# Optimization experiments

Measured on AMD Instinct MI355X. Metric: run time of the kernel, lower is better.

The kernel has to match this reference:

```python
import jax, jax.numpy as jnp
import numpy as np

ALPHA_BASE = 1.2
ALPHA_SCALE = 0.3
GRAPH_LAMBDA = 0.3
FUSION_BETA = 0.1
PRIOR_BETA = 0.2
LN_EPS = 1e-5  # nn.LayerNorm default

B, L, C = 8, 8192, 512
STAT, HID, GF, EMB = 4, 16, 16, 16


def _linear_params(key, out_d, in_d):
    kw, kb = jax.random.split(key)
    bound = 1.0 / np.sqrt(in_d)
    W = jax.random.uniform(kw, (out_d, in_d), minval=-bound, maxval=bound, dtype=jnp.float32)
    b = jax.random.uniform(kb, (out_d,), minval=-bound, maxval=bound, dtype=jnp.float32)
    return W, b


def setup_inputs() -> dict:
    key = jax.random.key(0)
    ks = jax.random.split(key, 9)
    residual = jax.random.normal(ks[0], (B, L, C), dtype=jnp.float32)
    node_embedding = jax.random.normal(ks[1], (C, EMB), dtype=jnp.float32) * 0.02
    W_l1, b_l1 = _linear_params(ks[2], HID, STAT)
    W_l2, b_l2 = _linear_params(ks[3], HID, HID)
    W_g, b_g = _linear_params(ks[4], HID, STAT)
    W_q, b_q = _linear_params(ks[5], GF, STAT)
    W_k, b_k = _linear_params(ks[6], GF, STAT)
    W_f, b_f = _linear_params(ks[7], HID, HID)
    W_o, b_o = _linear_params(ks[8], 1, HID)
    ln_g = jnp.ones((HID,), jnp.float32)
    ln_b = jnp.zeros((HID,), jnp.float32)
    return dict(residual=residual, node_embedding=node_embedding,
                W_l1=W_l1, b_l1=b_l1, W_l2=W_l2, b_l2=b_l2,
                W_g=W_g, b_g=b_g, W_q=W_q, b_q=b_q, W_k=W_k, b_k=b_k,
                W_f=W_f, b_f=b_f, W_o=W_o, b_o=b_o, ln_g=ln_g, ln_b=ln_b)


def reference(residual, node_embedding, W_l1, b_l1, W_l2, b_l2, W_g, b_g,
              W_q, b_q, W_k, b_k, W_f, b_f, W_o, b_o, ln_g, ln_b):
    # --- residual statistics: [B,L,C] -> [B,C,4] ---
    abs_res = jnp.abs(residual)
    m = abs_res.mean(axis=1)                       # mean(|r|)
    mx = abs_res.max(axis=1)                       # max(|r|)
    sq = (residual * residual).mean(axis=1)        # energy == mean(|r|^2)
    std = jnp.sqrt(jnp.maximum(sq - m * m, 0.0))   # biased std of |r|
    h0 = jnp.stack([m, mx, std, sq], axis=-1)      # [B,C,4]

    # --- local branch ---
    h_local = jax.nn.relu(h0 @ W_l1.T + b_l1) @ W_l2.T + b_l2  # [B,C,H]

    # --- adaptive adjacency ---
    q = h0 @ W_q.T + b_q                            # [B,C,G]
    k = h0 @ W_k.T + b_k                            # [B,C,G]
    sim_data = jax.nn.relu(jnp.einsum('bcg,bdg->bcd', q, k))
    sim_prior = jax.nn.relu(node_embedding @ node_embedding.T)  # [C,C]
    eye = jnp.eye(sim_data.shape[-1], dtype=sim_data.dtype)
    sim = sim_data + PRIOR_BETA * sim_prior[None] + eye[None]
    A = jax.nn.softmax(sim, axis=-1)                # [B,C,C]

    # --- message passing ---
    h_graph_in = h0 @ W_g.T + b_g                   # [B,C,H]
    msg = jnp.einsum('bcd,bdh->bch', A, h_graph_in)
    h_graph = h_graph_in + GRAPH_LAMBDA * jax.nn.relu(msg)

    # --- fusion + layernorm + head ---
    h = h_local + FUSION_BETA * h_graph
    mu = h.mean(axis=-1, keepdims=True)
    var = ((h - mu) ** 2).mean(axis=-1, keepdims=True)
    h = (h - mu) / jnp.sqrt(var + LN_EPS) * ln_g + ln_b
    h = jax.nn.relu(h @ W_f.T + b_f)
    delta = ALPHA_SCALE * jnp.tanh(h @ W_o.T + b_o)  # [B,C,1]
    alpha = (ALPHA_BASE + delta).transpose(0, 2, 1)  # [B,1,C]
    return alpha, h0, A
```

## Files before the change

kernel.cpp:

```cpp
#include <hip/hip_runtime.h>
#include <math.h>

#define BB 8
#define LL 8192
#define CC 512
#define NCH 64

#define H0_OFF (BB*CC)
#define A_OFF  (H0_OFF + BB*CC*4)

#define F_ALPHA_BASE 1.2f
#define F_ALPHA_SCALE 0.3f
#define F_GRAPH_LAMBDA 0.3f
#define F_FUSION_BETA 0.1f
#define F_PRIOR_BETA 0.2f
#define F_LN_EPS 1e-5f

struct P {
    const float* res; const float* ne;
    const float* Wl1; const float* bl1; const float* Wl2; const float* bl2;
    const float* Wg;  const float* bg;  const float* Wq;  const float* bq;
    const float* Wk;  const float* bk;  const float* Wf;  const float* bf;
    const float* Wo;  const float* bo;  const float* lng; const float* lnb;
    float* out; float* pbuf;
};

__global__ __launch_bounds__(256) void k_stats(P p) {
    __shared__ float smem[3 * CC];
    int b = blockIdx.x >> 6, cb = blockIdx.x & 63;
    int sub = threadIdx.x >> 7;
    int c4 = (threadIdx.x & 127) * 4;
    const float* base = p.res + ((size_t)b * LL + cb * 128 + sub * 64) * CC + c4;
    float s0 = 0.f, s1 = 0.f, s2 = 0.f, s3 = 0.f;
    float m0 = 0.f, m1 = 0.f, m2 = 0.f, m3 = 0.f;
    float q0 = 0.f, q1 = 0.f, q2 = 0.f, q3 = 0.f;
    #pragma unroll 8
    for (int r = 0; r < 64; r++) {
        float4 v = *(const float4*)(base + (size_t)r * CC);
        s0 += fabsf(v.x); s1 += fabsf(v.y); s2 += fabsf(v.z); s3 += fabsf(v.w);
        m0 = fmaxf(m0, fabsf(v.x)); m1 = fmaxf(m1, fabsf(v.y));
        m2 = fmaxf(m2, fabsf(v.z)); m3 = fmaxf(m3, fabsf(v.w));
        q0 = fmaf(v.x, v.x, q0); q1 = fmaf(v.y, v.y, q1);
        q2 = fmaf(v.z, v.z, q2); q3 = fmaf(v.w, v.w, q3);
    }
    if (sub == 1) {
        *(float4*)&smem[0 * CC + c4] = make_float4(s0, s1, s2, s3);
        *(float4*)&smem[1 * CC + c4] = make_float4(m0, m1, m2, m3);
        *(float4*)&smem[2 * CC + c4] = make_float4(q0, q1, q2, q3);
    }
    __syncthreads();
    if (sub == 0) {
        float4 cs = *(const float4*)&smem[0 * CC + c4];
        float4 cm = *(const float4*)&smem[1 * CC + c4];
        float4 cq = *(const float4*)&smem[2 * CC + c4];
        s0 += cs.x; s1 += cs.y; s2 += cs.z; s3 += cs.w;
        m0 = fmaxf(m0, cm.x); m1 = fmaxf(m1, cm.y);
        m2 = fmaxf(m2, cm.z); m3 = fmaxf(m3, cm.w);
        q0 += cq.x; q1 += cq.y; q2 += cq.z; q3 += cq.w;
        float* pb = p.pbuf + ((size_t)(b * 3) * NCH + cb) * CC + c4;
        *(float4*)(pb)                        = make_float4(s0, s1, s2, s3);
        *(float4*)(pb + (size_t)NCH * CC)     = make_float4(m0, m1, m2, m3);
        *(float4*)(pb + (size_t)2 * NCH * CC) = make_float4(q0, q1, q2, q3);
    }
}

__global__ __launch_bounds__(256) void k_rows(P p) {
    __shared__ float pl[4 * CC];
    __shared__ float stg[3 * CC];
    int tid = threadIdx.x;
    int b = blockIdx.x >> 6, rb = blockIdx.x & 63;
    int wid = tid >> 6, lane = tid & 63;
    int row0 = rb * 8 + wid * 2;

    int c4 = (tid & 127) * 4;
    int part = tid >> 7;
    const float* pS = p.pbuf + ((size_t)(b * 3 + 0) * NCH + part * 32) * CC + c4;
    const float* pM = p.pbuf + ((size_t)(b * 3 + 1) * NCH + part * 32) * CC + c4;
    const float* pQ = p.pbuf + ((size_t)(b * 3 + 2) * NCH + part * 32) * CC + c4;
    float as0 = 0.f, as1 = 0.f, as2 = 0.f, as3 = 0.f;
    float am0 = 0.f, am1 = 0.f, am2 = 0.f, am3 = 0.f;
    float aq0 = 0.f, aq1 = 0.f, aq2 = 0.f, aq3 = 0.f;
    #pragma unroll 8
    for (int i = 0; i < 32; i++) {
        float4 v = *(const float4*)(pS + (size_t)i * CC);
        as0 += v.x; as1 += v.y; as2 += v.z; as3 += v.w;
        float4 w = *(const float4*)(pM + (size_t)i * CC);
        am0 = fmaxf(am0, w.x); am1 = fmaxf(am1, w.y);
        am2 = fmaxf(am2, w.z); am3 = fmaxf(am3, w.w);
        float4 u = *(const float4*)(pQ + (size_t)i * CC);
        aq0 += u.x; aq1 += u.y; aq2 += u.z; aq3 += u.w;
    }
    if (part == 1) {
        *(float4*)&stg[0 * CC + c4] = make_float4(as0, as1, as2, as3);
        *(float4*)&stg[1 * CC + c4] = make_float4(am0, am1, am2, am3);
        *(float4*)&stg[2 * CC + c4] = make_float4(aq0, aq1, aq2, aq3);
    }

    float nr[2][16];
    #pragma unroll
    for (int rr = 0; rr < 2; rr++) {
        #pragma unroll
        for (int t = 0; t < 4; t++) {
            float4 v = *(const float4*)(p.ne + (size_t)(row0 + rr) * 16 + t * 4);
            nr[rr][4 * t] = v.x; nr[rr][4 * t + 1] = v.y;
            nr[rr][4 * t + 2] = v.z; nr[rr][4 * t + 3] = v.w;
        }
    }
    float pr0[8], pr1[8];
    #pragma unroll
    for (int j = 0; j < 8; j++) {
        int col = lane + 64 * j;
        float d0 = 0.f, d1 = 0.f;
        #pragma unroll
        for (int t = 0; t < 4; t++) {
            float4 v = *(const float4*)(p.ne + (size_t)col * 16 + t * 4);
            d0 = fmaf(nr[0][4 * t], v.x, d0); d0 = fmaf(nr[0][4 * t + 1], v.y, d0);
            d0 = fmaf(nr[0][4 * t + 2], v.z, d0); d0 = fmaf(nr[0][4 * t + 3], v.w, d0);
            d1 = fmaf(nr[1][4 * t], v.x, d1); d1 = fmaf(nr[1][4 * t + 1], v.y, d1);
            d1 = fmaf(nr[1][4 * t + 2], v.z, d1); d1 = fmaf(nr[1][4 * t + 3], v.w, d1);
        }
        pr0[j] = fmaxf(d0, 0.f);
        pr1[j] = fmaxf(d1, 0.f);
    }

    __syncthreads();
    if (part == 0) {
        float4 cs = *(const float4*)&stg[0 * CC + c4];
        float4 cm = *(const float4*)&stg[1 * CC + c4];
        float4 cq = *(const float4*)&stg[2 * CC + c4];
        float S[4] = {as0 + cs.x, as1 + cs.y, as2 + cs.z, as3 + cs.w};
        float M[4] = {fmaxf(am0, cm.x), fmaxf(am1, cm.y), fmaxf(am2, cm.z), fmaxf(am3, cm.w)};
        float Q[4] = {aq0 + cq.x, aq1 + cq.y, aq2 + cq.z, aq3 + cq.w};
        #pragma unroll
        for (int k = 0; k < 4; k++) {
            float m = S[k] * (1.f / LL);
            float sqm = Q[k] * (1.f / LL);
            float sd = sqrtf(fmaxf(sqm - m * m, 0.f));
            int col = c4 + k;
            pl[col] = m;
            pl[CC + col] = M[k];
            pl[2 * CC + col] = sd;
            pl[3 * CC + col] = sqm;
            if (rb == 0)
                *(float4*)(p.out + H0_OFF + ((size_t)b * CC + col) * 4) =
                    make_float4(m, M[k], sd, sqm);
        }
    }
    __syncthreads();

    float sloc[2][4], u[2][4], c0[2];
    #pragma unroll
    for (int rr = 0; rr < 2; rr++) {
        int row = row0 + rr;
        float sv0 = pl[row], sv1 = pl[CC + row];
        float sv2 = pl[2 * CC + row], sv3 = pl[3 * CC + row];
        sloc[rr][0] = sv0; sloc[rr][1] = sv1; sloc[rr][2] = sv2; sloc[rr][3] = sv3;
        float uu0 = 0.f, uu1 = 0.f, uu2 = 0.f, uu3 = 0.f, cc = 0.f;
        #pragma unroll
        for (int i = 0; i < 16; i++) {
            float qi = p.bq[i];
            qi = fmaf(p.Wq[i * 4 + 0], sv0, qi);
            qi = fmaf(p.Wq[i * 4 + 1], sv1, qi);
            qi = fmaf(p.Wq[i * 4 + 2], sv2, qi);
            qi = fmaf(p.Wq[i * 4 + 3], sv3, qi);
            uu0 = fmaf(qi, p.Wk[i * 4 + 0], uu0);
            uu1 = fmaf(qi, p.Wk[i * 4 + 1], uu1);
            uu2 = fmaf(qi, p.Wk[i * 4 + 2], uu2);
            uu3 = fmaf(qi, p.Wk[i * 4 + 3], uu3);
            cc = fmaf(qi, p.bk[i], cc);
        }
        u[rr][0] = uu0; u[rr][1] = uu1; u[rr][2] = uu2; u[rr][3] = uu3;
        c0[rr] = cc;
    }

    float sv[2][8];
    float mx0 = -1e30f, mx1 = -1e30f;
    #pragma unroll
    for (int j = 0; j < 8; j++) {
        int col = lane + 64 * j;
        float h0c = pl[col], h1c = pl[CC + col];
        float h2c = pl[2 * CC + col], h3c = pl[3 * CC + col];
        float d0 = c0[0], d1 = c0[1];
        d0 = fmaf(u[0][0], h0c, d0); d1 = fmaf(u[1][0], h0c, d1);
        d0 = fmaf(u[0][1], h1c, d0); d1 = fmaf(u[1][1], h1c, d1);
        d0 = fmaf(u[0][2], h2c, d0); d1 = fmaf(u[1][2], h2c, d1);
        d0 = fmaf(u[0][3], h3c, d0); d1 = fmaf(u[1][3], h3c, d1);
        float v0 = fmaxf(d0, 0.f) + F_PRIOR_BETA * pr0[j] + (col == row0 ? 1.f : 0.f);
        float v1 = fmaxf(d1, 0.f) + F_PRIOR_BETA * pr1[j] + (col == row0 + 1 ? 1.f : 0.f);
        sv[0][j] = v0; sv[1][j] = v1;
        mx0 = fmaxf(mx0, v0); mx1 = fmaxf(mx1, v1);
    }
    #pragma unroll
    for (int o = 32; o; o >>= 1) {
        mx0 = fmaxf(mx0, __shfl_xor(mx0, o));
        mx1 = fmaxf(mx1, __shfl_xor(mx1, o));
    }

    float ls0 = 0.f, ls1 = 0.f;
    float T0[4] = {0.f, 0.f, 0.f, 0.f}, T1[4] = {0.f, 0.f, 0.f, 0.f};
    #pragma unroll
    for (int j = 0; j < 8; j++) {
        int col = lane + 64 * j;
        float e0 = expf(sv[0][j] - mx0);
        float e1 = expf(sv[1][j] - mx1);
        sv[0][j] = e0; sv[1][j] = e1;
        ls0 += e0; ls1 += e1;
        float h0c = pl[col], h1c = pl[CC + col];
        float h2c = pl[2 * CC + col], h3c = pl[3 * CC + col];
        T0[0] = fmaf(e0, h0c, T0[0]); T1[0] = fmaf(e1, h0c, T1[0]);
        T0[1] = fmaf(e0, h1c, T0[1]); T1[1] = fmaf(e1, h1c, T1[1]);
        T0[2] = fmaf(e0, h2c, T0[2]); T1[2] = fmaf(e1, h2c, T1[2]);
        T0[3] = fmaf(e0, h3c, T0[3]); T1[3] = fmaf(e1, h3c, T1[3]);
    }
    #pragma unroll
    for (int o = 32; o; o >>= 1) {
        ls0 += __shfl_xor(ls0, o); ls1 += __shfl_xor(ls1, o);
        T0[0] += __shfl_xor(T0[0], o); T1[0] += __shfl_xor(T1[0], o);
        T0[1] += __shfl_xor(T0[1], o); T1[1] += __shfl_xor(T1[1], o);
        T0[2] += __shfl_xor(T0[2], o); T1[2] += __shfl_xor(T1[2], o);
        T0[3] += __shfl_xor(T0[3], o); T1[3] += __shfl_xor(T1[3], o);
    }
    float inv0 = 1.f / ls0, inv1 = 1.f / ls1;

    float* arow = p.out + A_OFF + ((size_t)b * CC + row0) * CC;
    #pragma unroll
    for (int j = 0; j < 8; j++) {
        arow[lane + 64 * j]      = sv[0][j] * inv0;
        arow[CC + lane + 64 * j] = sv[1][j] * inv1;
    }

    int rr = lane >> 5;
    float inv = rr ? inv1 : inv0;
    float Ta = (rr ? T1[0] : T0[0]) * inv;
    float Tb = (rr ? T1[1] : T0[1]) * inv;
    float Tc = (rr ? T1[2] : T0[2]) * inv;
    float Td = (rr ? T1[3] : T0[3]) * inv;
    float s20 = rr ? sloc[1][0] : sloc[0][0];
    float s21 = rr ? sloc[1][1] : sloc[0][1];
    float s22 = rr ? sloc[1][2] : sloc[0][2];
    float s23 = rr ? sloc[1][3] : sloc[0][3];

    float gcomb[16];
    #pragma unroll
    for (int h = 0; h < 16; h++) {
        float w0 = p.Wg[h * 4 + 0], w1 = p.Wg[h * 4 + 1];
        float w2 = p.Wg[h * 4 + 2], w3 = p.Wg[h * 4 + 3];
        float bgh = p.bg[h];
        float hg = bgh;
        hg = fmaf(w0, s20, hg); hg = fmaf(w1, s21, hg);
        hg = fmaf(w2, s22, hg); hg = fmaf(w3, s23, hg);
        float mg = bgh;
        mg = fmaf(w0, Ta, mg); mg = fmaf(w1, Tb, mg);
        mg = fmaf(w2, Tc, mg); mg = fmaf(w3, Td, mg);
        gcomb[h] = hg + F_GRAPH_LAMBDA * fmaxf(mg, 0.f);
    }
    float t1v[16];
    #pragma unroll
    for (int i = 0; i < 16; i++) {
        float a = p.bl1[i];
        a = fmaf(p.Wl1[i * 4 + 0], s20, a);
        a = fmaf(p.Wl1[i * 4 + 1], s21, a);
        a = fmaf(p.Wl1[i * 4 + 2], s22, a);
        a = fmaf(p.Wl1[i * 4 + 3], s23, a);
        t1v[i] = fmaxf(a, 0.f);
    }
    float hvec[16];
    float mu = 0.f;
    #pragma unroll
    for (int h = 0; h < 16; h++) {
        float hl = p.bl2[h];
        #pragma unroll
        for (int j = 0; j < 16; j++) hl = fmaf(p.Wl2[h * 16 + j], t1v[j], hl);
        float hv = hl + F_FUSION_BETA * gcomb[h];
        hvec[h] = hv;
        mu += hv;
    }
    mu *= (1.f / 16.f);
    float var = 0.f;
    #pragma unroll
    for (int h = 0; h < 16; h++) { float d = hvec[h] - mu; var = fmaf(d, d, var); }
    var *= (1.f / 16.f);
    float istd = 1.f / sqrtf(var + F_LN_EPS);
    float hn[16];
    #pragma unroll
    for (int h = 0; h < 16; h++) hn[h] = (hvec[h] - mu) * istd * p.lng[h] + p.lnb[h];

    float acc2 = p.bo[0];
    #pragma unroll
    for (int o = 0; o < 16; o++) {
        float f = p.bf[o];
        #pragma unroll
        for (int t = 0; t < 16; t++) f = fmaf(p.Wf[o * 16 + t], hn[t], f);
        acc2 = fmaf(p.Wo[o], fmaxf(f, 0.f), acc2);
    }
    float alpha = F_ALPHA_BASE + F_ALPHA_SCALE * tanhf(acc2);
    if ((lane & 31) == 0) p.out[(size_t)b * CC + row0 + rr] = alpha;
}

extern "C" void kernel_launch(void* const* d_in, const int* in_sizes, int n_in,
                              void* d_out, int out_size, void* d_ws, size_t ws_size,
                              hipStream_t stream) {
    P p;
    p.res = (const float*)d_in[0];
    p.ne  = (const float*)d_in[1];
    p.Wl1 = (const float*)d_in[2];
    p.bl1 = (const float*)d_in[3];
    p.Wl2 = (const float*)d_in[4];
    p.bl2 = (const float*)d_in[5];
    p.Wg  = (const float*)d_in[6];
    p.bg  = (const float*)d_in[7];
    p.Wq  = (const float*)d_in[8];
    p.bq  = (const float*)d_in[9];
    p.Wk  = (const float*)d_in[10];
    p.bk  = (const float*)d_in[11];
    p.Wf  = (const float*)d_in[12];
    p.bf  = (const float*)d_in[13];
    p.Wo  = (const float*)d_in[14];
    p.bo  = (const float*)d_in[15];
    p.lng = (const float*)d_in[16];
    p.lnb = (const float*)d_in[17];
    p.out  = (float*)d_out;
    p.pbuf = (float*)d_ws;

    k_stats<<<BB * NCH, 256, 0, stream>>>(p);
    k_rows<<<BB * 64, 256, 0, stream>>>(p);
}
```

Measured before the change: 55.73 us.

## Hoist partial-stat reduction into a separate kernel shared by all row blocks

Adds a small k_red kernel that reduces the per-chunk sum/max/sumsq partials once per batch and channel, computes h0, and writes it to the output and a workspace buffer. k_rows now loads the precomputed h0 instead of each of its 64 blocks per batch redundantly re-reducing all partials. This removes heavy redundant L2/global reads at the cost of an extra kernel launch and a serial dependency.

```diff
diff --git a/kernel.cpp b/kernel.cpp
--- a/kernel.cpp
+++ b/kernel.cpp
@@ -22,7 +22,7 @@
     const float* Wg;  const float* bg;  const float* Wq;  const float* bq;
     const float* Wk;  const float* bk;  const float* Wf;  const float* bf;
     const float* Wo;  const float* bo;  const float* lng; const float* lnb;
-    float* out; float* pbuf;
+    float* out; float* pbuf; float* h0ws;
 };
 
 __global__ __launch_bounds__(256) void k_stats(P p) {
@@ -64,36 +64,55 @@
     }
 }
 
+__global__ __launch_bounds__(256) void k_red(P p) {
+    __shared__ float red[4][3][64];
+    int w = threadIdx.x >> 6, lane = threadIdx.x & 63;
+    int b = blockIdx.x >> 3;
+    int c = (blockIdx.x & 7) * 64 + lane;
+    const float* pS = p.pbuf + ((size_t)(b * 3 + 0) * NCH + w * 16) * CC + c;
+    const float* pM = p.pbuf + ((size_t)(b * 3 + 1) * NCH + w * 16) * CC + c;
+    const float* pQ = p.pbuf + ((size_t)(b * 3 + 2) * NCH + w * 16) * CC + c;
+    float sum = 0.f, mx = 0.f, sq = 0.f;
+    #pragma unroll
+    for (int i = 0; i < 16; i++) {
+        sum += pS[(size_t)i * CC];
+        mx = fmaxf(mx, pM[(size_t)i * CC]);
+        sq += pQ[(size_t)i * CC];
+    }
+    red[w][0][lane] = sum;
+    red[w][1][lane] = mx;
+    red[w][2][lane] = sq;
+    __syncthreads();
+    if (w == 0) {
+        float ts = red[0][0][lane] + red[1][0][lane] + red[2][0][lane] + red[3][0][lane];
+        float tm = fmaxf(fmaxf(red[0][1][lane], red[1][1][lane]),
+                         fmaxf(red[2][1][lane], red[3][1][lane]));
+        float tq = red[0][2][lane] + red[1][2][lane] + red[2][2][lane] + red[3][2][lane];
+        float m = ts * (1.f / LL);
+        float sqm = tq * (1.f / LL);
+        float sd = sqrtf(fmaxf(sqm - m * m, 0.f));
+        float4 h0v = make_float4(m, tm, sd, sqm);
+        size_t g = (size_t)b * CC + c;
+        *(float4*)(p.h0ws + g * 4) = h0v;
+        *(float4*)(p.out + H0_OFF + g * 4) = h0v;
+    }
+}
+
 __global__ __launch_bounds__(256) void k_rows(P p) {
     __shared__ float pl[4 * CC];
-    __shared__ float stg[3 * CC];
     int tid = threadIdx.x;
     int b = blockIdx.x >> 6, rb = blockIdx.x & 63;
     int wid = tid >> 6, lane = tid & 63;
     int row0 = rb * 8 + wid * 2;
 
-    int c4 = (tid & 127) * 4;
-    int part = tid >> 7;
-    const float* pS = p.pbuf + ((size_t)(b * 3 + 0) * NCH + part * 32) * CC + c4;
-    const float* pM = p.pbuf + ((size_t)(b * 3 + 1) * NCH + part * 32) * CC + c4;
-    const float* pQ = p.pbuf + ((size_t)(b * 3 + 2) * NCH + part * 32) * CC + c4;
-    float as0 = 0.f, as1 = 0.f, as2 = 0.f, as3 = 0.f;
-    float am0 = 0.f, am1 = 0.f, am2 = 0.f, am3 = 0.f;
-    float aq0 = 0.f, aq1 = 0.f, aq2 = 0.f, aq3 = 0.f;
-    #pragma unroll 8
-    for (int i = 0; i < 32; i++) {
-        float4 v = *(const float4*)(pS + (size_t)i * CC);
-        as0 += v.x; as1 += v.y; as2 += v.z; as3 += v.w;
-        float4 w = *(const float4*)(pM + (size_t)i * CC);
-        am0 = fmaxf(am0, w.x); am1 = fmaxf(am1, w.y);
-        am2 = fmaxf(am2, w.z); am3 = fmaxf(am3, w.w);
-        float4 u = *(const float4*)(pQ + (size_t)i * CC);
-        aq0 += u.x; aq1 += u.y; aq2 += u.z; aq3 += u.w;
-    }
-    if (part == 1) {
-        *(float4*)&stg[0 * CC + c4] = make_float4(as0, as1, as2, as3);
-        *(float4*)&stg[1 * CC + c4] = make_float4(am0, am1, am2, am3);
-        *(float4*)&stg[2 * CC + c4] = make_float4(aq0, aq1, aq2, aq3);
+    #pragma unroll
+    for (int ccy = 0; ccy < 2; ccy++) {
+        int col = tid + ccy * 256;
+        float4 hv = *(const float4*)(p.h0ws + ((size_t)b * CC + col) * 4);
+        pl[col] = hv.x;
+        pl[CC + col] = hv.y;
+        pl[2 * CC + col] = hv.z;
+        pl[3 * CC + col] = hv.w;
     }
 
     float nr[2][16];
@@ -121,30 +140,6 @@
         }
         pr0[j] = fmaxf(d0, 0.f);
         pr1[j] = fmaxf(d1, 0.f);
-    }
-
-    __syncthreads();
-    if (part == 0) {
-        float4 cs = *(const float4*)&stg[0 * CC + c4];
-        float4 cm = *(const float4*)&stg[1 * CC + c4];
-        float4 cq = *(const float4*)&stg[2 * CC + c4];
-        float S[4] = {as0 + cs.x, as1 + cs.y, as2 + cs.z, as3 + cs.w};
-        float M[4] = {fmaxf(am0, cm.x), fmaxf(am1, cm.y), fmaxf(am2, cm.z), fmaxf(am3, cm.w)};
-        float Q[4] = {aq0 + cq.x, aq1 + cq.y, aq2 + cq.z, aq3 + cq.w};
-        #pragma unroll
-        for (int k = 0; k < 4; k++) {
-            float m = S[k] * (1.f / LL);
-            float sqm = Q[k] * (1.f / LL);
-            float sd = sqrtf(fmaxf(sqm - m * m, 0.f));
-            int col = c4 + k;
-            pl[col] = m;
-            pl[CC + col] = M[k];
-            pl[2 * CC + col] = sd;
-            pl[3 * CC + col] = sqm;
-            if (rb == 0)
-                *(float4*)(p.out + H0_OFF + ((size_t)b * CC + col) * 4) =
-                    make_float4(m, M[k], sd, sqm);
-        }
     }
     __syncthreads();
 
@@ -321,7 +316,9 @@
     p.lnb = (const float*)d_in[17];
     p.out  = (float*)d_out;
     p.pbuf = (float*)d_ws;
+    p.h0ws = (float*)d_ws + (size_t)BB * 3 * NCH * CC;
 
     k_stats<<<BB * NCH, 256, 0, stream>>>(p);
+    k_red<<<64, 256, 0, stream>>>(p);
     k_rows<<<BB * 64, 256, 0, stream>>>(p);
 }
```

Result: faster. 50.05 us (-10.2%).
